# Kernel optimization log

Measured on AMD Instinct MI355X. Metric: run time of the kernel, lower is better.

Reference implementation:

```python
import jax, jax.numpy as jnp
import numpy as np

N, C, H, W = 32, 512, 56, 56
R = 16            # reduction
F = 8             # num_split frequencies
MAPPER_X = [0, 0, 1, -1, 0, 3, 0, 2]
MAPPER_Y = [0, 1, 0, -1, 3, 0, 2, 0]


def _dct_filters():
    # FcaNet DCT basis: cos(pi*freq*(pos+0.5)/POS)/sqrt(POS), *sqrt(2) if freq != 0
    def basis(freq, POS):
        pos = np.arange(POS, dtype=np.float64)
        r = np.cos(np.pi * freq * (pos + 0.5) / POS) / np.sqrt(POS)
        if freq != 0:
            r = r * np.sqrt(2.0)
        return r

    filt = np.zeros((F, H, W), dtype=np.float32)
    for f, (u, v) in enumerate(zip(MAPPER_X, MAPPER_Y)):
        filt[f] = np.outer(basis(u, H), basis(v, W)).astype(np.float32)
    return jnp.asarray(filt)


def setup_inputs() -> dict:
    key = jax.random.key(0)
    kx, k1, k2 = jax.random.split(key, 3)
    x = jax.random.normal(kx, (N, C, H, W), dtype=jnp.float32)
    dct = _dct_filters()                                   # (F, H, W) fixed buffer
    # grouped Conv1d(C*F -> C//R*F, k=1, groups=F): per-group weight (C//R, C)
    w1 = jax.random.normal(k1, (F, C // R, C), dtype=jnp.float32) * (1.0 / np.sqrt(C))
    # Conv1d(C//R*F -> C, k=1): weight (C, F, C//R)
    w2 = jax.random.normal(k2, (C, F, C // R), dtype=jnp.float32) * (1.0 / np.sqrt(F * C // R))
    return {"x": x, "dct": dct, "w1": w1, "w2": w2}


def reference(x, dct, w1, w2):
    # Multi-frequency DCT pooling: one pass over x, 8 weighted spatial sums -> (n, F, c)
    y = jnp.einsum('nchw,fhw->nfc', x, dct)
    # Grouped 1x1 Conv1d (groups=F) + ReLU: per-frequency squeeze -> (n, F, c//R)
    z = jax.nn.relu(jnp.einsum('nfc,foc->nfo', y, w1))
    # Full-mix 1x1 Conv1d + Sigmoid -> (n, c)
    s = jax.nn.sigmoid(jnp.einsum('nfo,cfo->nc', z, w2))
    # Broadcast channel scale
    return x * s[:, :, None, None]
```

## Files before the change

### kernel.cpp

```cpp
#include <hip/hip_runtime.h>
#include <cstddef>

#define NB   32
#define CH   512
#define HHW  3136
#define HW4  784
#define FF   8
#define CR   32
#define CIT  2

typedef float f4v __attribute__((ext_vector_type(4)));

__global__ __launch_bounds__(256, 4)
void pool_kernel(const float* __restrict__ x,
                 const float* __restrict__ dct,
                 float* __restrict__ y ) {
    __shared__ float4 bht[60];
    __shared__ float4 bwt[14][4];

    const int t = threadIdx.x;
    const float SQ = 7.4833147735478827f;
    if (t < 56) {
        bht[t] = make_float4(dct[0*HHW + t*56] * SQ,
                             dct[2*HHW + t*56] * SQ,
                             dct[7*HHW + t*56] * SQ,
                             dct[5*HHW + t*56] * SQ);
    } else if (t < 60) {
        bht[t] = make_float4(0.f, 0.f, 0.f, 0.f);
    } else if (t >= 64 && t < 120) {
        const int i = t - 64, wc = i >> 2, p = i & 3;
        const int FP[4] = {0, 1, 6, 4};
        const float4 v = *(const float4*)(dct + (size_t)FP[p]*HHW + wc*4);
        bwt[wc][p] = make_float4(v.x*SQ, v.y*SQ, v.z*SQ, v.w*SQ);
    }
    __syncthreads();

    const int lane = t & 63, wave = t >> 6;
    const int r  = lane / 14;
    const int wc = lane % 14;
    const int lx = lane < 56 ? lane : 55;
    const float zf = lane < 56 ? 1.f : 0.f;
    float4 bw0 = bwt[wc][0], bw1 = bwt[wc][1], bw2 = bwt[wc][2], bw3 = bwt[wc][3];
    bw0.x*=zf; bw0.y*=zf; bw0.z*=zf; bw0.w*=zf;
    bw1.x*=zf; bw1.y*=zf; bw1.z*=zf; bw1.w*=zf;
    bw2.x*=zf; bw2.y*=zf; bw2.z*=zf; bw2.w*=zf;
    bw3.x*=zf; bw3.y*=zf; bw3.z*=zf; bw3.w*=zf;

    const int gc0 = blockIdx.x * (4*CIT) + wave * CIT;

    for (int it = 0; it < CIT; ++it) {
        const int gc = gc0 + it;
        const float4* xb = (const float4*)(x + (size_t)gc * HHW);
        float acc[8] = {0.f,0.f,0.f,0.f,0.f,0.f,0.f,0.f};
        #pragma unroll
        for (int j = 0; j < 14; ++j) {
            const float4 xv = xb[j*56 + lx];
            const float4 bh = bht[4*j + r];
            const float s0 = xv.x*bw0.x + xv.y*bw0.y + xv.z*bw0.z + xv.w*bw0.w;
            const float s1 = xv.x*bw1.x + xv.y*bw1.y + xv.z*bw1.z + xv.w*bw1.w;
            const float s2 = xv.x*bw2.x + xv.y*bw2.y + xv.z*bw2.z + xv.w*bw2.w;
            const float s3 = xv.x*bw3.x + xv.y*bw3.y + xv.z*bw3.z + xv.w*bw3.w;
            acc[0] += bh.x * s0;
            acc[1] += bh.x * s1;
            acc[2] += bh.y * s0;
            acc[3] += bh.y * s1;
            acc[4] += bh.x * s3;
            acc[5] += bh.w * s0;
            acc[6] += bh.x * s2;
            acc[7] += bh.z * s0;
        }

#define RSTEP(S, HALF)                                              \
        {                                                           \
            const bool hi = (lane >> (S)) & 1;                      \
            _Pragma("unroll")                                       \
            for (int k = 0; k < (HALF); ++k) {                      \
                float send = hi ? acc[k] : acc[k + (HALF)];         \
                float recv = __shfl_xor(send, 1 << (S), 64);        \
                acc[k] = (hi ? acc[k + (HALF)] : acc[k]) + recv;    \
            }                                                       \
        }
        RSTEP(0, 4) RSTEP(1, 2) RSTEP(2, 1)
#undef RSTEP
        acc[0] += __shfl_xor(acc[0], 8, 64);
        acc[0] += __shfl_xor(acc[0], 16, 64);
        acc[0] += __shfl_xor(acc[0], 32, 64);

        if (lane < 8) {
            const int f = ((lane & 1) << 2) | (lane & 2) | ((lane >> 2) & 1);
            y[(size_t)(gc >> 9) * (FF*CH) + (size_t)f * CH + (gc & (CH-1))] = acc[0];
        }
    }
}

__global__ void excite_kernel(const float* __restrict__ y  ,
                              const float* __restrict__ w1 ,
                              const float* __restrict__ w2 ,
                              float* __restrict__ s        ) {
    const int n = blockIdx.x;
    __shared__ __align__(16) float zl[FF * CR];

    const int f = threadIdx.x >> 5, o = threadIdx.x & 31;
    const float4* yr = (const float4*)(y + (size_t)n * FF * CH + (size_t)f * CH);
    const float4* wr = (const float4*)(w1 + ((size_t)(f * CR + o)) * CH);
    float a = 0.f;
    #pragma unroll 8
    for (int j = 0; j < CH/4; ++j) {
        float4 yv = yr[j], wv = wr[j];
        a += yv.x*wv.x + yv.y*wv.y + yv.z*wv.z + yv.w*wv.w;
    }
    zl[threadIdx.x] = a > 0.f ? a : 0.f;
    __syncthreads();

    #pragma unroll
    for (int cc = 0; cc < 2; ++cc) {
        const int c = threadIdx.x + 256 * cc;
        const float4* w2r = (const float4*)(w2 + (size_t)c * FF * CR);
        const float4* zr  = (const float4*)zl;
        float b = 0.f;
        #pragma unroll 8
        for (int k = 0; k < FF*CR/4; ++k) {
            float4 wv = w2r[k], zv = zr[k];
            b += wv.x*zv.x + wv.y*zv.y + wv.z*zv.z + wv.w*zv.w;
        }
        s[(size_t)n * CH + c] = 1.f / (1.f + __expf(-b));
    }
}

__global__ void scale_kernel(const float* __restrict__ x,
                             const float* __restrict__ s,
                             float* __restrict__ out) {
    const int ch   = blockIdx.x * 4 + (threadIdx.x >> 6);
    const int lane = threadIdx.x & 63;
    const float sv = s[ch];
    const f4v* xb = (const f4v*)(x + (size_t)ch * HHW);
    f4v*       ob = (f4v*)(out + (size_t)ch * HHW);
    for (int i = lane; i < HW4; i += 64) {
        f4v v = xb[i] * sv;
        __builtin_nontemporal_store(v, ob + i);
    }
}

extern "C" void kernel_launch(void* const* d_in, const int* in_sizes, int n_in,
                              void* d_out, int out_size, void* d_ws, size_t ws_size,
                              hipStream_t stream) {
    const float* x   = (const float*)d_in[0];
    const float* dct = (const float*)d_in[1];
    const float* w1  = (const float*)d_in[2];
    const float* w2  = (const float*)d_in[3];
    float* out = (float*)d_out;

    float* y = (float*)d_ws;
    float* s = y + (size_t)NB * FF * CH;

    pool_kernel  <<<(NB*CH)/(4*CIT), 256, 0, stream>>>(x, dct, y);
    excite_kernel<<<NB,              256, 0, stream>>>(y, w1, w2, s);
    scale_kernel <<<NB * (CH / 4),   256, 0, stream>>>(x, s, out);
}
```

Measured before the change: 419.0 us.

## Fuse excitation MLP into channel-scale kernel with per-block redundant squeeze

Merges the excite and scale kernels so that each 1024-thread block loads the pooled vector of its sample, recomputes the grouped squeeze layer, and computes sigmoid gates for its 16 channels before scaling them. This removes a kernel launch and the poorly parallel 32-block excite stage along with its round trip through workspace. In exchange, every block redundantly reads all of w1 (512KB), which adds heavy L2 traffic. The nontemporal store on the output was also replaced with ordinary stores.

```diff
diff --git a/kernel.cpp b/kernel.cpp
--- a/kernel.cpp
+++ b/kernel.cpp
@@ -93,51 +93,59 @@
     }
 }
 
-__global__ void excite_kernel(const float* __restrict__ y  ,
-                              const float* __restrict__ w1 ,
-                              const float* __restrict__ w2 ,
-                              float* __restrict__ s        ) {
-    const int n = blockIdx.x;
+__global__ __launch_bounds__(1024, 8)
+void excite_scale_kernel(const float* __restrict__ x,
+                         const float* __restrict__ y  ,
+                         const float* __restrict__ w1 ,
+                         const float* __restrict__ w2 ,
+                         float* __restrict__ out) {
+    const int n  = blockIdx.x >> 5;
+    const int cb = blockIdx.x & 31;
+    const int t  = threadIdx.x;
+
+    __shared__ __align__(16) float yl[FF * CH];
     __shared__ __align__(16) float zl[FF * CR];
 
-    const int f = threadIdx.x >> 5, o = threadIdx.x & 31;
-    const float4* yr = (const float4*)(y + (size_t)n * FF * CH + (size_t)f * CH);
-    const float4* wr = (const float4*)(w1 + ((size_t)(f * CR + o)) * CH);
-    float a = 0.f;
-    #pragma unroll 8
-    for (int j = 0; j < CH/4; ++j) {
-        float4 yv = yr[j], wv = wr[j];
-        a += yv.x*wv.x + yv.y*wv.y + yv.z*wv.z + yv.w*wv.w;
-    }
-    zl[threadIdx.x] = a > 0.f ? a : 0.f;
+    ((float4*)yl)[t] = ((const float4*)(y + (size_t)n * FF * CH))[t];
     __syncthreads();
 
-    #pragma unroll
-    for (int cc = 0; cc < 2; ++cc) {
-        const int c = threadIdx.x + 256 * cc;
-        const float4* w2r = (const float4*)(w2 + (size_t)c * FF * CR);
-        const float4* zr  = (const float4*)zl;
-        float b = 0.f;
+    {
+        const int fo = t >> 2, p = t & 3;
+        const float4* yr = (const float4*)yl + (size_t)(fo >> 5) * (CH/4);
+        const float4* wr = (const float4*)(w1 + (size_t)fo * CH);
+        float a = 0.f;
         #pragma unroll 8
-        for (int k = 0; k < FF*CR/4; ++k) {
-            float4 wv = w2r[k], zv = zr[k];
-            b += wv.x*zv.x + wv.y*zv.y + wv.z*zv.z + wv.w*zv.w;
+        for (int j = 0; j < 32; ++j) {
+            const float4 yv = yr[p + 4*j];
+            const float4 wv = wr[p + 4*j];
+            a += yv.x*wv.x + yv.y*wv.y + yv.z*wv.z + yv.w*wv.w;
         }
-        s[(size_t)n * CH + c] = 1.f / (1.f + __expf(-b));
+        a += __shfl_xor(a, 1, 64);
+        a += __shfl_xor(a, 2, 64);
+        if (p == 0) zl[fo] = a > 0.f ? a : 0.f;
     }
-}
+    __syncthreads();
 
-__global__ void scale_kernel(const float* __restrict__ x,
-                             const float* __restrict__ s,
-                             float* __restrict__ out) {
-    const int ch   = blockIdx.x * 4 + (threadIdx.x >> 6);
-    const int lane = threadIdx.x & 63;
-    const float sv = s[ch];
-    const f4v* xb = (const f4v*)(x + (size_t)ch * HHW);
-    f4v*       ob = (f4v*)(out + (size_t)ch * HHW);
+    const int w = t >> 6, lane = t & 63;
+    const int c = cb * 16 + w;
+    const float4 zv = ((const float4*)zl)[lane];
+    const float4 wv = ((const float4*)(w2 + (size_t)c * FF * CR))[lane];
+    float a = zv.x*wv.x + zv.y*wv.y + zv.z*wv.z + zv.w*wv.w;
+    a += __shfl_xor(a, 1, 64);
+    a += __shfl_xor(a, 2, 64);
+    a += __shfl_xor(a, 4, 64);
+    a += __shfl_xor(a, 8, 64);
+    a += __shfl_xor(a, 16, 64);
+    a += __shfl_xor(a, 32, 64);
+    const float sv = 1.f / (1.f + __expf(-a));
+
+    const int ch = n * CH + c;
+    const float4* xb = (const float4*)(x + (size_t)ch * HHW);
+    float4*       ob = (float4*)(out + (size_t)ch * HHW);
     for (int i = lane; i < HW4; i += 64) {
-        f4v v = xb[i] * sv;
-        __builtin_nontemporal_store(v, ob + i);
+        float4 v = xb[i];
+        v.x *= sv; v.y *= sv; v.z *= sv; v.w *= sv;
+        ob[i] = v;
     }
 }
 
@@ -151,9 +159,7 @@
     float* out = (float*)d_out;
 
     float* y = (float*)d_ws;
-    float* s = y + (size_t)NB * FF * CH;
 
-    pool_kernel  <<<(NB*CH)/(4*CIT), 256, 0, stream>>>(x, dct, y);
-    excite_kernel<<<NB,              256, 0, stream>>>(y, w1, w2, s);
-    scale_kernel <<<NB * (CH / 4),   256, 0, stream>>>(x, s, out);
+    pool_kernel        <<<(NB*CH)/(4*CIT), 256,  0, stream>>>(x, dct, y);
+    excite_scale_kernel<<<NB * 32,         1024, 0, stream>>>(x, y, w1, w2, out);
 }
```

New measurement: 405.8 us. 1.03x faster.
